# Kernel optimization log

Hardware: AMD Instinct MI355X
Metric: run time of the kernel (lower is better)

Reference implementation:

```python
import jax, jax.numpy as jnp
import numpy as np

B, S, E, H, I = 32, 257, 1024, 16, 4096
D = E // H  # head_dim = 64
EPS = 1e-5


def setup_inputs() -> dict:
    key = jax.random.key(0)
    ks = jax.random.split(key, 12)
    std = 0.02
    inp = {
        'hidden_states': jax.random.normal(ks[0], (B, S, E), jnp.float32),
        'attention_mask': jnp.zeros((B, 1, S, S), jnp.float32),
        'causal_attention_mask': jnp.zeros((B, 1, S, S), jnp.float32),
        'ln1_w': jnp.ones((E,), jnp.float32),
        'ln1_b': jnp.zeros((E,), jnp.float32),
        'q_w': jax.random.normal(ks[1], (E, E), jnp.float32) * std,
        'q_b': jnp.zeros((E,), jnp.float32),
        'k_w': jax.random.normal(ks[2], (E, E), jnp.float32) * std,
        'k_b': jnp.zeros((E,), jnp.float32),
        'v_w': jax.random.normal(ks[3], (E, E), jnp.float32) * std,
        'v_b': jnp.zeros((E,), jnp.float32),
        'o_w': jax.random.normal(ks[4], (E, E), jnp.float32) * std,
        'o_b': jnp.zeros((E,), jnp.float32),
        'ln2_w': jnp.ones((E,), jnp.float32),
        'ln2_b': jnp.zeros((E,), jnp.float32),
        'fc1_w': jax.random.normal(ks[5], (I, E), jnp.float32) * std,
        'fc1_b': jnp.zeros((I,), jnp.float32),
        'fc2_w': jax.random.normal(ks[6], (E, I), jnp.float32) * std,
        'fc2_b': jnp.zeros((E,), jnp.float32),
    }
    return inp


def _layernorm(x, w, b):
    mu = jnp.mean(x, axis=-1, keepdims=True)
    var = jnp.mean(jnp.square(x - mu), axis=-1, keepdims=True)
    return (x - mu) * jax.lax.rsqrt(var + EPS) * w + b


def _gelu_tanh(x):
    # 0.5*x*(1+tanh(sqrt(2/pi)*(x+0.044715*x^3)))
    c = np.sqrt(2.0 / np.pi).astype(np.float32)
    return 0.5 * x * (1.0 + jnp.tanh(c * (x + 0.044715 * x * x * x)))


def reference(hidden_states, attention_mask, causal_attention_mask,
              ln1_w, ln1_b, q_w, q_b, k_w, k_b, v_w, v_b, o_w, o_b,
              ln2_w, ln2_b, fc1_w, fc1_b, fc2_w, fc2_b):
    scale = D ** -0.5
    residual = hidden_states
    x = _layernorm(hidden_states, ln1_w, ln1_b)

    # projections (torch Linear: x @ W.T + b), q pre-scaled as in source
    q = (x @ q_w.T + q_b) * scale
    k = x @ k_w.T + k_b
    v = x @ v_w.T + v_b

    # [B, H, S, D]
    q = q.reshape(B, S, H, D).transpose(0, 2, 1, 3)
    k = k.reshape(B, S, H, D).transpose(0, 2, 1, 3)
    v = v.reshape(B, S, H, D).transpose(0, 2, 1, 3)

    scores = jnp.einsum('bhqd,bhkd->bhqk', q, k)  # [B,H,S,S]
    scores = scores + causal_attention_mask + attention_mask
    probs = jax.nn.softmax(scores, axis=-1)
    ctx = jnp.einsum('bhqk,bhkd->bhqd', probs, v)
    ctx = ctx.transpose(0, 2, 1, 3).reshape(B, S, E)
    attn_out = ctx @ o_w.T + o_b

    h = residual + attn_out
    residual = h
    x = _layernorm(h, ln2_w, ln2_b)
    x = _gelu_tanh(x @ fc1_w.T + fc1_b)
    x = x @ fc2_w.T + fc2_b
    return residual + x
```

## Files before the change

kernel.cpp:

```cpp
#include <hip/hip_runtime.h>

typedef unsigned short u16;
typedef unsigned int   u32;
typedef short s16x8 __attribute__((ext_vector_type(8)));
typedef float f32x4 __attribute__((ext_vector_type(4)));

#define MFMA16(A,B,C) __builtin_amdgcn_mfma_f32_16x16x32_bf16((A),(B),(C),0,0,0)

#define B_   32
#define S_   257
#define E_   1024
#define H_   16
#define D_   64
#define I_   4096
#define M_   (B_*S_)

__device__ __forceinline__ u16 f2bf(float f) {
    u32 u = __float_as_uint(f);
    u32 r = u + 0x7fffu + ((u >> 16) & 1u);
    return (u16)(r >> 16);
}
__device__ __forceinline__ float bf2f(u16 b) {
    return __uint_as_float(((u32)b) << 16);
}

__device__ __forceinline__ void gload16(const void* g, void* l) {
    __builtin_amdgcn_global_load_lds(
        (const __attribute__((address_space(1))) u32*)g,
        (__attribute__((address_space(3))) u32*)l, 16, 0, 0);
}

__global__ __launch_bounds__(256)
void convert_w_kernel(const float* __restrict__ qw, const float* __restrict__ kw,
                      const float* __restrict__ vw, const float* __restrict__ ow,
                      const float* __restrict__ f1, const float* __restrict__ f2,
                      u16* __restrict__ dst)
{
    const int total4 = (12 * 1048576) / 4;
    for (int i = blockIdx.x * 256 + threadIdx.x; i < total4; i += gridDim.x * 256) {
        int e = i * 4;
        int seg = e >> 20;
        const float* srcp; int off;
        if (seg < 4)      { srcp = (seg == 0 ? qw : seg == 1 ? kw : seg == 2 ? vw : ow); off = e & 1048575; }
        else if (seg < 8) { srcp = f1; off = e - 4 * 1048576; }
        else              { srcp = f2; off = e - 8 * 1048576; }
        float4 v = *(const float4*)(srcp + off);
        ushort4 o;
        o.x = f2bf(v.x); o.y = f2bf(v.y); o.z = f2bf(v.z); o.w = f2bf(v.w);
        *(ushort4*)(dst + e) = o;
    }
}

__global__ __launch_bounds__(256)
void mask_combine_kernel(const float* __restrict__ am, const float* __restrict__ cm,
                         u16* __restrict__ msum)
{
    const int total = B_ * S_ * 272;
    for (int i = blockIdx.x * 256 + threadIdx.x; i < total; i += gridDim.x * 256) {
        int skv = i % 272;
        int rem = i / 272;
        int sq  = rem % S_;
        int b   = rem / S_;
        float v;
        if (skv < S_) {
            size_t o = ((size_t)b * S_ + sq) * S_ + skv;
            v = am[o] + cm[o];
        } else v = -1e30f;
        msum[i] = f2bf(v);
    }
}

__global__ __launch_bounds__(256)
void ln_kernel(const float* __restrict__ src, const float* __restrict__ gam,
               const float* __restrict__ bet, u16* __restrict__ dst)
{
    int row = blockIdx.x;
    const float4* p = (const float4*)(src + (size_t)row * E_);
    float4 x = p[threadIdx.x];
    float s  = x.x + x.y + x.z + x.w;
    float s2 = x.x * x.x + x.y * x.y + x.z * x.z + x.w * x.w;
#pragma unroll
    for (int xm = 1; xm < 64; xm <<= 1) {
        s  += __shfl_xor(s,  xm, 64);
        s2 += __shfl_xor(s2, xm, 64);
    }
    __shared__ float red[8];
    int wv = threadIdx.x >> 6;
    if ((threadIdx.x & 63) == 0) { red[wv] = s; red[4 + wv] = s2; }
    __syncthreads();
    s  = red[0] + red[1] + red[2] + red[3];
    s2 = red[4] + red[5] + red[6] + red[7];
    float mu  = s * (1.0f / 1024.0f);
    float var = s2 * (1.0f / 1024.0f) - mu * mu;
    float rs  = rsqrtf(var + 1e-5f);
    float4 g  = ((const float4*)gam)[threadIdx.x];
    float4 be = ((const float4*)bet)[threadIdx.x];
    ushort4 o;
    o.x = f2bf((x.x - mu) * rs * g.x + be.x);
    o.y = f2bf((x.y - mu) * rs * g.y + be.y);
    o.z = f2bf((x.z - mu) * rs * g.z + be.z);
    o.w = f2bf((x.w - mu) * rs * g.w + be.w);
    ((ushort4*)dst)[(size_t)row * 256 + threadIdx.x] = o;
}

template<int MODE>
__global__ __launch_bounds__(256)
void gemm_bt(const u16* __restrict__ A,
             const u16* __restrict__ B0, const u16* __restrict__ B1, const u16* __restrict__ B2,
             const float* __restrict__ bias0, const float* __restrict__ bias1, const float* __restrict__ bias2,
             const float* __restrict__ res, float* __restrict__ outF,
             u16* __restrict__ outB0, u16* __restrict__ outB1, u16* __restrict__ outB2,
             int M, int N, int K)
{
    __shared__ u16 As[128 * 32];
    __shared__ u16 Bs[128 * 32];
    const int tid = threadIdx.x, lane = tid & 63, wv = tid >> 6;
    const int mt = blockIdx.y;
    const u16* Bm = B0; const float* bias = bias0; u16* outB = outB0;
    float scl = 1.0f;
    int nt = blockIdx.x;
    if (MODE == 0) {
        int mat = nt >> 3; nt &= 7;
        if (mat == 1)      { Bm = B1; bias = bias1; outB = outB1; }
        else if (mat == 2) { Bm = B2; bias = bias2; outB = outB2; }
        if (mat == 0) scl = 0.125f;
    }
    const int m0 = mt * 128, n0 = nt * 128;
    const int lr = lane & 15, lg = lane >> 4;
    const int wm = wv >> 1, wn = wv & 1;

    f32x4 acc[4][4];
#pragma unroll
    for (int i = 0; i < 4; ++i)
#pragma unroll
        for (int j = 0; j < 4; ++j) { f32x4 z = {0.f, 0.f, 0.f, 0.f}; acc[i][j] = z; }

    for (int k0 = 0; k0 < K; k0 += 32) {
#pragma unroll
        for (int i = 0; i < 2; ++i) {
            int c  = i * 256 + tid;
            int r  = c >> 2, cc = (c & 3) << 3;
            int ra = m0 + r; if (ra > M - 1) ra = M - 1;
            gload16(A  + (size_t)ra * K + k0 + cc, As + (i * 256 + wv * 64) * 8);
            gload16(Bm + (size_t)(n0 + r) * K + k0 + cc, Bs + (i * 256 + wv * 64) * 8);
        }
        __syncthreads();
        s16x8 af[4], bfr[4];
#pragma unroll
        for (int f = 0; f < 4; ++f) {
            af[f]  = *(const s16x8*)&As[(wm * 64 + f * 16 + lr) * 32 + lg * 8];
            bfr[f] = *(const s16x8*)&Bs[(wn * 64 + f * 16 + lr) * 32 + lg * 8];
        }
#pragma unroll
        for (int fm = 0; fm < 4; ++fm)
#pragma unroll
            for (int fn = 0; fn < 4; ++fn)
                acc[fm][fn] = MFMA16(af[fm], bfr[fn], acc[fm][fn]);
        __syncthreads();
    }

    float biasv[4];
#pragma unroll
    for (int fn = 0; fn < 4; ++fn) biasv[fn] = bias[n0 + wn * 64 + fn * 16 + lr];

#pragma unroll
    for (int fm = 0; fm < 4; ++fm) {
#pragma unroll
        for (int r = 0; r < 4; ++r) {
            int row = m0 + wm * 64 + fm * 16 + lg * 4 + r;
            if (row >= M) continue;
            if (MODE == 0) {
                int bb = row / S_;
                int ss = row - bb * S_;
#pragma unroll
                for (int fn = 0; fn < 4; ++fn) {
                    int col = n0 + wn * 64 + fn * 16 + lr;
                    int hh = col >> 6, dd = col & 63;
                    float v = (acc[fm][fn][r] + biasv[fn]) * scl;
                    outB[(((size_t)bb * H_ + hh) * S_ + ss) * D_ + dd] = f2bf(v);
                }
            } else if (MODE == 1) {
                size_t base = (size_t)row * N;
#pragma unroll
                for (int fn = 0; fn < 4; ++fn) {
                    int col = n0 + wn * 64 + fn * 16 + lr;
                    outF[base + col] = acc[fm][fn][r] + biasv[fn] + res[base + col];
                }
            } else {
                size_t base = (size_t)row * N;
#pragma unroll
                for (int fn = 0; fn < 4; ++fn) {
                    int col = n0 + wn * 64 + fn * 16 + lr;
                    float x = acc[fm][fn][r] + biasv[fn];
                    float u = 0.7978845608028654f * (x + 0.044715f * x * x * x);
                    float t = tanhf(u);
                    outB[base + col] = f2bf(0.5f * x * (1.0f + t));
                }
            }
        }
    }
}

__global__ __launch_bounds__(256)
void attn_kernel(const u16* __restrict__ qg_, const u16* __restrict__ kg_,
                 const u16* __restrict__ vg_, const u16* __restrict__ msum,
                 u16* __restrict__ ctx)
{
    __shared__ u16 Ks[272 * 72];
    __shared__ u16 Vt[64 * 296];
    __shared__ u16 Ps[4][16 * 32];
    const int bh = blockIdx.x;
    const int b = bh >> 4, hh = bh & 15;
    const u16* kg = kg_ + (size_t)bh * (S_ * D_);
    const u16* vg = vg_ + (size_t)bh * (S_ * D_);
    const u16* qg = qg_ + (size_t)bh * (S_ * D_);
    const int tid = threadIdx.x, lane = tid & 63, wv = tid >> 6;

    for (int c = tid; c < (S_ * D_) / 8; c += 256) {
        int s = c >> 3, d8 = (c & 7) << 3;
        s16x8 val = *(const s16x8*)(kg + s * 64 + d8);
        *(s16x8*)&Ks[s * 72 + d8] = val;
    }
    for (int idx = tid; idx < 15 * 64; idx += 256) {
        int rr = 257 + (idx >> 6), cc = idx & 63;
        Ks[rr * 72 + cc] = 0;
    }
    for (int c = tid; c < (S_ * D_) / 8; c += 256) {
        int s = c >> 3, d8 = (c & 7) << 3;
        s16x8 val = *(const s16x8*)(vg + s * 64 + d8);
#pragma unroll
        for (int j = 0; j < 8; ++j) Vt[(d8 + j) * 296 + s] = (u16)val[j];
    }
    for (int idx = tid; idx < 64 * 39; idx += 256) {
        int dd = idx / 39, cc = 257 + idx % 39;
        Vt[dd * 296 + cc] = 0;
    }
    __syncthreads();

    const int lr = lane & 15, lg = lane >> 4;
    for (int qb = wv; qb < 17; qb += 4) {
        const int q0 = qb * 16;
        int qrow = q0 + lr; if (qrow > S_ - 1) qrow = S_ - 1;
        s16x8 aq0 = *(const s16x8*)(qg + qrow * 64 + lg * 8);
        s16x8 aq1 = *(const s16x8*)(qg + qrow * 64 + 32 + lg * 8);

        f32x4 sc[17];
#pragma unroll
        for (int t = 0; t < 17; ++t) { f32x4 z = {0.f, 0.f, 0.f, 0.f}; sc[t] = z; }
#pragma unroll
        for (int t = 0; t < 17; ++t) {
            s16x8 b0 = *(const s16x8*)&Ks[(t * 16 + lr) * 72 + lg * 8];
            s16x8 b1 = *(const s16x8*)&Ks[(t * 16 + lr) * 72 + 32 + lg * 8];
            sc[t] = MFMA16(aq0, b0, sc[t]);
            sc[t] = MFMA16(aq1, b1, sc[t]);
        }
        float mx[4] = {-3e38f, -3e38f, -3e38f, -3e38f};
#pragma unroll
        for (int r = 0; r < 4; ++r) {
            int sq = q0 + lg * 4 + r; if (sq > S_ - 1) sq = S_ - 1;
            const u16* mrow = msum + ((size_t)b * S_ + sq) * 272;
#pragma unroll
            for (int t = 0; t < 17; ++t) {
                sc[t][r] += bf2f(mrow[t * 16 + lr]);
                mx[r] = fmaxf(mx[r], sc[t][r]);
            }
        }
#pragma unroll
        for (int r = 0; r < 4; ++r) {
#pragma unroll
            for (int xm = 1; xm <= 8; xm <<= 1)
                mx[r] = fmaxf(mx[r], __shfl_xor(mx[r], xm, 64));
        }
        float sum[4] = {0.f, 0.f, 0.f, 0.f};
#pragma unroll
        for (int t = 0; t < 17; ++t)
#pragma unroll
            for (int r = 0; r < 4; ++r) {
                float e = __expf(sc[t][r] - mx[r]);
                sc[t][r] = e; sum[r] += e;
            }
#pragma unroll
        for (int r = 0; r < 4; ++r) {
#pragma unroll
            for (int xm = 1; xm <= 8; xm <<= 1)
                sum[r] += __shfl_xor(sum[r], xm, 64);
        }

        f32x4 ac[4];
#pragma unroll
        for (int nt = 0; nt < 4; ++nt) { f32x4 z = {0.f, 0.f, 0.f, 0.f}; ac[nt] = z; }
        u16* myP = &Ps[wv][0];
#pragma unroll
        for (int kc = 0; kc < 9; ++kc) {
#pragma unroll
            for (int tt = 0; tt < 2; ++tt) {
                const int t = kc * 2 + tt;
#pragma unroll
                for (int r = 0; r < 4; ++r) {
                    float pv = (t < 17) ? sc[(t < 17) ? t : 0][r] : 0.f;
                    myP[(lg * 4 + r) * 32 + tt * 16 + lr] = f2bf(pv);
                }
            }
            s16x8 pa = *(const s16x8*)&myP[lr * 32 + lg * 8];
#pragma unroll
            for (int nt = 0; nt < 4; ++nt) {
                s16x8 bv = *(const s16x8*)&Vt[(nt * 16 + lr) * 296 + kc * 32 + lg * 8];
                ac[nt] = MFMA16(pa, bv, ac[nt]);
            }
        }
#pragma unroll
        for (int r = 0; r < 4; ++r) {
            int sq = q0 + lg * 4 + r;
            if (sq < S_) {
                float rd = 1.0f / sum[r];
                size_t base = (((size_t)b * S_ + sq) * H_ + hh) * D_;
#pragma unroll
                for (int nt = 0; nt < 4; ++nt)
                    ctx[base + nt * 16 + lr] = f2bf(ac[nt][r] * rd);
            }
        }
    }
}

extern "C" void kernel_launch(void* const* d_in, const int* in_sizes, int n_in,
                              void* d_out, int out_size, void* d_ws, size_t ws_size,
                              hipStream_t stream)
{
    const float* hid   = (const float*)d_in[0];
    const float* am    = (const float*)d_in[1];
    const float* cm    = (const float*)d_in[2];
    const float* ln1w  = (const float*)d_in[3];
    const float* ln1b  = (const float*)d_in[4];
    const float* qw    = (const float*)d_in[5];
    const float* qbias = (const float*)d_in[6];
    const float* kw    = (const float*)d_in[7];
    const float* kbias = (const float*)d_in[8];
    const float* vw    = (const float*)d_in[9];
    const float* vbias = (const float*)d_in[10];
    const float* ow    = (const float*)d_in[11];
    const float* obias = (const float*)d_in[12];
    const float* ln2w  = (const float*)d_in[13];
    const float* ln2b  = (const float*)d_in[14];
    const float* f1w   = (const float*)d_in[15];
    const float* f1b   = (const float*)d_in[16];
    const float* f2w   = (const float*)d_in[17];
    const float* f2b   = (const float*)d_in[18];
    float* out = (float*)d_out;

    const size_t ME = (size_t)M_ * E_;
    u16* Wq   = (u16*)d_ws;
    u16* Wk   = Wq + 1048576;
    u16* Wv   = Wk + 1048576;
    u16* Wo   = Wv + 1048576;
    u16* Wf1  = Wo + 1048576;
    u16* Wf2  = Wf1 + 4 * 1048576;
    u16* xln  = Wf2 + 4 * 1048576;
    u16* qb_  = xln + ME;
    u16* kb_  = qb_ + ME;
    u16* vb_  = kb_ + ME;
    u16* ctx  = vb_ + ME;
    float* hbuf = (float*)(ctx + ME);
    u16* msum = (u16*)(hbuf + ME);
    u16* act  = qb_;
    u16* x2   = xln;

    convert_w_kernel<<<3072, 256, 0, stream>>>(qw, kw, vw, ow, f1w, f2w, Wq);
    mask_combine_kernel<<<8736, 256, 0, stream>>>(am, cm, msum);
    ln_kernel<<<M_, 256, 0, stream>>>(hid, ln1w, ln1b, xln);
    gemm_bt<0><<<dim3(24, 65), 256, 0, stream>>>(xln, Wq, Wk, Wv, qbias, kbias, vbias,
                                                 nullptr, nullptr, qb_, kb_, vb_,
                                                 M_, E_, E_);
    attn_kernel<<<512, 256, 0, stream>>>(qb_, kb_, vb_, msum, ctx);
    gemm_bt<1><<<dim3(8, 65), 256, 0, stream>>>(ctx, Wo, nullptr, nullptr, obias, nullptr, nullptr,
                                                hid, hbuf, nullptr, nullptr, nullptr,
                                                M_, E_, E_);
    ln_kernel<<<M_, 256, 0, stream>>>(hbuf, ln2w, ln2b, x2);
    gemm_bt<2><<<dim3(32, 65), 256, 0, stream>>>(x2, Wf1, nullptr, nullptr, f1b, nullptr, nullptr,
                                                 nullptr, nullptr, act, nullptr, nullptr,
                                                 M_, I_, E_);
    gemm_bt<1><<<dim3(8, 65), 256, 0, stream>>>(act, Wf2, nullptr, nullptr, f2b, nullptr, nullptr,
                                                hbuf, out, nullptr, nullptr, nullptr,
                                                M_, E_, I_);
}
```

Before: 461.4 us.

## Replace GEMM with 256x256-tile 8-wave kernel using double-buffered swizzled LDS pipeline

Replaces the 128x128 single-buffered GEMM with a 512-thread kernel computing 256x256 tiles. Global-to-LDS loads for the next K step are interleaved with MFMA phases through a double buffer, with explicit waitcnt, barriers and setprio. LDS addresses are XOR-swizzled to cut bank conflicts. The intent is to raise data reuse per load and hide memory latency behind matrix math. In exchange it uses many more registers (32 accumulators per wave) and leaves a coarser grid with more padding waste on the M edge (8224 rows in 33 tiles of 256).

```diff
diff --git a/kernel.cpp b/kernel.cpp
--- a/kernel.cpp
+++ b/kernel.cpp
@@ -6,6 +6,7 @@
 typedef float f32x4 __attribute__((ext_vector_type(4)));
 
 #define MFMA16(A,B,C) __builtin_amdgcn_mfma_f32_16x16x32_bf16((A),(B),(C),0,0,0)
+#define BAR() asm volatile("s_barrier" ::: "memory")
 
 #define B_   32
 #define S_   257
@@ -104,94 +105,159 @@
 }
 
 template<int MODE>
-__global__ __launch_bounds__(256)
-void gemm_bt(const u16* __restrict__ A,
-             const u16* __restrict__ B0, const u16* __restrict__ B1, const u16* __restrict__ B2,
-             const float* __restrict__ bias0, const float* __restrict__ bias1, const float* __restrict__ bias2,
-             const float* __restrict__ res, float* __restrict__ outF,
-             u16* __restrict__ outB0, u16* __restrict__ outB1, u16* __restrict__ outB2,
-             int M, int N, int K)
-{
-    __shared__ u16 As[128 * 32];
-    __shared__ u16 Bs[128 * 32];
-    const int tid = threadIdx.x, lane = tid & 63, wv = tid >> 6;
+__global__ __launch_bounds__(512, 2)
+void gemm8(const u16* __restrict__ A,
+           const u16* __restrict__ Bq, const u16* __restrict__ Bk, const u16* __restrict__ Bv,
+           const float* __restrict__ biasq, const float* __restrict__ biask, const float* __restrict__ biasvv,
+           const float* __restrict__ res, float* __restrict__ outF,
+           u16* __restrict__ outBq, u16* __restrict__ outBk, u16* __restrict__ outBv,
+           int M, int N, int K)
+{
+    __shared__ u16 lds[8][4096];
+    const int tid  = threadIdx.x;
+    const int lane = tid & 63, w = tid >> 6;
+    const int lr = lane & 15, lg = lane >> 4;
+    const int wm = w >> 2, wn = w & 3;
     const int mt = blockIdx.y;
-    const u16* Bm = B0; const float* bias = bias0; u16* outB = outB0;
-    float scl = 1.0f;
-    int nt = blockIdx.x;
+
+    const u16* Bm = Bq; const float* bias = biasq; u16* outB = outBq;
+    float scl = 1.0f; int nt = blockIdx.x;
     if (MODE == 0) {
-        int mat = nt >> 3; nt &= 7;
-        if (mat == 1)      { Bm = B1; bias = bias1; outB = outB1; }
-        else if (mat == 2) { Bm = B2; bias = bias2; outB = outB2; }
+        int mat = nt >> 2; nt &= 3;
+        if (mat == 1)      { Bm = Bk; bias = biask; outB = outBk; }
+        else if (mat == 2) { Bm = Bv; bias = biasvv; outB = outBv; }
         if (mat == 0) scl = 0.125f;
     }
-    const int m0 = mt * 128, n0 = nt * 128;
-    const int lr = lane & 15, lg = lane >> 4;
-    const int wm = wv >> 1, wn = wv & 1;
-
-    f32x4 acc[4][4];
-#pragma unroll
-    for (int i = 0; i < 4; ++i)
+    const int m0 = mt * 256, n0 = nt * 256;
+    const int NT = K >> 5;
+
+    auto STAGE = [&](const u16* g, int grow0, int rowmax, int kt, int mat, int h) {
+        char* dst = (char*)&lds[((kt & 1) << 2) + (mat << 1) + h][0] + w * 1024;
+        int p = (w * 64 + lane) << 4;
+        int l = p ^ (((p >> 7) & 3) << 4);
+        int row = l >> 6, cc = (l >> 4) & 3;
+        int gr = grow0 + row; if (gr > rowmax) gr = rowmax;
+        gload16(g + (size_t)gr * K + (kt << 5) + cc * 8, dst);
+    };
+    const int swv = ((lr >> 1) & 3) << 4;
+    auto LDA = [&](int kt, int mh, int mf) -> s16x8 {
+        const char* base = (const char*)&lds[((kt & 1) << 2) + wm][0];
+        return *(const s16x8*)(base + (mh * 64 + mf * 16 + lr) * 64 + ((lg * 16) ^ swv));
+    };
+    auto LDB = [&](int kt, int nh, int nf) -> s16x8 {
+        const char* base = (const char*)&lds[((kt & 1) << 2) + 2 + (wn >> 1)][0];
+        return *(const s16x8*)(base + ((wn & 1) * 64 + nh * 32 + nf * 16 + lr) * 64 + ((lg * 16) ^ swv));
+    };
+
+    f32x4 acc[8][4];
+#pragma unroll
+    for (int i = 0; i < 8; ++i)
 #pragma unroll
         for (int j = 0; j < 4; ++j) { f32x4 z = {0.f, 0.f, 0.f, 0.f}; acc[i][j] = z; }
 
-    for (int k0 = 0; k0 < K; k0 += 32) {
-#pragma unroll
-        for (int i = 0; i < 2; ++i) {
-            int c  = i * 256 + tid;
-            int r  = c >> 2, cc = (c & 3) << 3;
-            int ra = m0 + r; if (ra > M - 1) ra = M - 1;
-            gload16(A  + (size_t)ra * K + k0 + cc, As + (i * 256 + wv * 64) * 8);
-            gload16(Bm + (size_t)(n0 + r) * K + k0 + cc, Bs + (i * 256 + wv * 64) * 8);
-        }
-        __syncthreads();
-        s16x8 af[4], bfr[4];
-#pragma unroll
-        for (int f = 0; f < 4; ++f) {
-            af[f]  = *(const s16x8*)&As[(wm * 64 + f * 16 + lr) * 32 + lg * 8];
-            bfr[f] = *(const s16x8*)&Bs[(wn * 64 + f * 16 + lr) * 32 + lg * 8];
-        }
-#pragma unroll
-        for (int fm = 0; fm < 4; ++fm)
-#pragma unroll
-            for (int fn = 0; fn < 4; ++fn)
-                acc[fm][fn] = MFMA16(af[fm], bfr[fn], acc[fm][fn]);
-        __syncthreads();
+    STAGE(A,  m0,       M - 1, 0, 0, 0);
+    STAGE(A,  m0 + 128, M - 1, 0, 0, 1);
+    STAGE(Bm, n0,       N - 1, 0, 1, 0);
+    STAGE(Bm, n0 + 128, N - 1, 0, 1, 1);
+    if (NT > 1) {
+        STAGE(A, m0, M - 1, 1, 0, 0);
+        asm volatile("s_waitcnt vmcnt(1)" ::: "memory");
+    } else {
+        asm volatile("s_waitcnt vmcnt(0)" ::: "memory");
+    }
+    BAR();
+
+    s16x8 aq[4], b0q[2], b1q[2];
+    for (int kt = 0; kt < NT; ++kt) {
+#pragma unroll
+        for (int mf = 0; mf < 4; ++mf) aq[mf] = LDA(kt, 0, mf);
+#pragma unroll
+        for (int nf = 0; nf < 2; ++nf) b0q[nf] = LDB(kt, 0, nf);
+        if (kt + 1 < NT) {
+            STAGE(A,  m0 + 128, M - 1, kt + 1, 0, 1);
+            STAGE(Bm, n0,       N - 1, kt + 1, 1, 0);
+        }
+        BAR();
+        __builtin_amdgcn_s_setprio(1);
+#pragma unroll
+        for (int mf = 0; mf < 4; ++mf)
+#pragma unroll
+            for (int nf = 0; nf < 2; ++nf)
+                acc[mf][nf] = MFMA16(aq[mf], b0q[nf], acc[mf][nf]);
+        __builtin_amdgcn_s_setprio(0);
+        BAR();
+#pragma unroll
+        for (int nf = 0; nf < 2; ++nf) b1q[nf] = LDB(kt, 1, nf);
+        if (kt + 1 < NT) STAGE(Bm, n0 + 128, N - 1, kt + 1, 1, 1);
+        BAR();
+        __builtin_amdgcn_s_setprio(1);
+#pragma unroll
+        for (int mf = 0; mf < 4; ++mf)
+#pragma unroll
+            for (int nf = 0; nf < 2; ++nf)
+                acc[mf][2 + nf] = MFMA16(aq[mf], b1q[nf], acc[mf][2 + nf]);
+        __builtin_amdgcn_s_setprio(0);
+        BAR();
+#pragma unroll
+        for (int mf = 0; mf < 4; ++mf) aq[mf] = LDA(kt, 1, mf);
+        BAR();
+        __builtin_amdgcn_s_setprio(1);
+#pragma unroll
+        for (int mf = 0; mf < 4; ++mf)
+#pragma unroll
+            for (int nf = 0; nf < 2; ++nf)
+                acc[4 + mf][2 + nf] = MFMA16(aq[mf], b1q[nf], acc[4 + mf][2 + nf]);
+        __builtin_amdgcn_s_setprio(0);
+        BAR();
+        if (kt + 2 < NT) STAGE(A, m0, M - 1, kt + 2, 0, 0);
+        BAR();
+        __builtin_amdgcn_s_setprio(1);
+#pragma unroll
+        for (int mf = 0; mf < 4; ++mf)
+#pragma unroll
+            for (int nf = 0; nf < 2; ++nf)
+                acc[4 + mf][nf] = MFMA16(aq[mf], b0q[nf], acc[4 + mf][nf]);
+        __builtin_amdgcn_s_setprio(0);
+        if (kt + 1 < NT) {
+            if (kt + 2 < NT) asm volatile("s_waitcnt vmcnt(1)" ::: "memory");
+            else             asm volatile("s_waitcnt vmcnt(0)" ::: "memory");
+        }
+        BAR();
     }
 
     float biasv[4];
 #pragma unroll
-    for (int fn = 0; fn < 4; ++fn) biasv[fn] = bias[n0 + wn * 64 + fn * 16 + lr];
-
-#pragma unroll
-    for (int fm = 0; fm < 4; ++fm) {
+    for (int an = 0; an < 4; ++an) biasv[an] = bias[n0 + wn * 64 + an * 16 + lr];
+
+#pragma unroll
+    for (int am = 0; am < 8; ++am) {
 #pragma unroll
         for (int r = 0; r < 4; ++r) {
-            int row = m0 + wm * 64 + fm * 16 + lg * 4 + r;
+            int row = m0 + wm * 128 + am * 16 + lg * 4 + r;
             if (row >= M) continue;
             if (MODE == 0) {
                 int bb = row / S_;
                 int ss = row - bb * S_;
 #pragma unroll
-                for (int fn = 0; fn < 4; ++fn) {
-                    int col = n0 + wn * 64 + fn * 16 + lr;
+                for (int an = 0; an < 4; ++an) {
+                    int col = n0 + wn * 64 + an * 16 + lr;
                     int hh = col >> 6, dd = col & 63;
-                    float v = (acc[fm][fn][r] + biasv[fn]) * scl;
+                    float v = (acc[am][an][r] + biasv[an]) * scl;
                     outB[(((size_t)bb * H_ + hh) * S_ + ss) * D_ + dd] = f2bf(v);
                 }
             } else if (MODE == 1) {
                 size_t base = (size_t)row * N;
 #pragma unroll
-                for (int fn = 0; fn < 4; ++fn) {
-                    int col = n0 + wn * 64 + fn * 16 + lr;
-                    outF[base + col] = acc[fm][fn][r] + biasv[fn] + res[base + col];
+                for (int an = 0; an < 4; ++an) {
+                    int col = n0 + wn * 64 + an * 16 + lr;
+                    outF[base + col] = acc[am][an][r] + biasv[an] + res[base + col];
                 }
             } else {
                 size_t base = (size_t)row * N;
 #pragma unroll
-                for (int fn = 0; fn < 4; ++fn) {
-                    int col = n0 + wn * 64 + fn * 16 + lr;
-                    float x = acc[fm][fn][r] + biasv[fn];
+                for (int an = 0; an < 4; ++an) {
+                    int col = n0 + wn * 64 + an * 16 + lr;
+                    float x = acc[am][an][r] + biasv[an];
                     float u = 0.7978845608028654f * (x + 0.044715f * x * x * x);
                     float t = tanhf(u);
                     outB[base + col] = f2bf(0.5f * x * (1.0f + t));
@@ -367,18 +433,18 @@
     convert_w_kernel<<<3072, 256, 0, stream>>>(qw, kw, vw, ow, f1w, f2w, Wq);
     mask_combine_kernel<<<8736, 256, 0, stream>>>(am, cm, msum);
     ln_kernel<<<M_, 256, 0, stream>>>(hid, ln1w, ln1b, xln);
-    gemm_bt<0><<<dim3(24, 65), 256, 0, stream>>>(xln, Wq, Wk, Wv, qbias, kbias, vbias,
-                                                 nullptr, nullptr, qb_, kb_, vb_,
-                                                 M_, E_, E_);
+    gemm8<0><<<dim3(12, 33), 512, 0, stream>>>(xln, Wq, Wk, Wv, qbias, kbias, vbias,
+                                               nullptr, nullptr, qb_, kb_, vb_,
+                                               M_, 1024, 1024);
     attn_kernel<<<512, 256, 0, stream>>>(qb_, kb_, vb_, msum, ctx);
-    gemm_bt<1><<<dim3(8, 65), 256, 0, stream>>>(ctx, Wo, nullptr, nullptr, obias, nullptr, nullptr,
-                                                hid, hbuf, nullptr, nullptr, nullptr,
-                                                M_, E_, E_);
+    gemm8<1><<<dim3(4, 33), 512, 0, stream>>>(ctx, Wo, nullptr, nullptr, obias, nullptr, nullptr,
+                                              hid, hbuf, nullptr, nullptr, nullptr,
+                                              M_, 1024, 1024);
     ln_kernel<<<M_, 256, 0, stream>>>(hbuf, ln2w, ln2b, x2);
-    gemm_bt<2><<<dim3(32, 65), 256, 0, stream>>>(x2, Wf1, nullptr, nullptr, f1b, nullptr, nullptr,
-                                                 nullptr, nullptr, act, nullptr, nullptr,
-                                                 M_, I_, E_);
-    gemm_bt<1><<<dim3(8, 65), 256, 0, stream>>>(act, Wf2, nullptr, nullptr, f2b, nullptr, nullptr,
-                                                hbuf, out, nullptr, nullptr, nullptr,
-                                                M_, E_, I_);
-}
+    gemm8<2><<<dim3(16, 33), 512, 0, stream>>>(x2, Wf1, nullptr, nullptr, f1b, nullptr, nullptr,
+                                               nullptr, nullptr, act, nullptr, nullptr,
+                                               M_, 4096, 1024);
+    gemm8<1><<<dim3(4, 33), 512, 0, stream>>>(act, Wf2, nullptr, nullptr, f2b, nullptr, nullptr,
+                                              hbuf, out, nullptr, nullptr, nullptr,
+                                              M_, 1024, 4096);
+}
```

Measured after the change: 464.4 us. Within noise of the previous version (+0.7%).

## Rewrite GEMMs with 256x256 tiles, double-buffered LDS, swizzle and XCD remap

Applied to the files above, without the earlier changes.

Replaces the 128x128 single-buffered GEMM with a 512-thread kernel that uses 256x256 output tiles, prefetches K-tiles two steps ahead into double-buffered LDS with explicit vmcnt waits, and XOR-swizzles LDS addresses to reduce bank conflicts. Workgroup IDs are remapped so that consecutive tiles land on the same XCD, which should improve L2 reuse. The GELU epilogue swaps tanhf for an exp-based sigmoid form. The goal is more data reuse per loaded byte and overlap of global loads with MFMA work, at the cost of higher register pressure and fewer workgroups.

```diff
diff --git a/kernel.cpp b/kernel.cpp
--- a/kernel.cpp
+++ b/kernel.cpp
@@ -6,6 +6,9 @@
 typedef float f32x4 __attribute__((ext_vector_type(4)));
 
 #define MFMA16(A,B,C) __builtin_amdgcn_mfma_f32_16x16x32_bf16((A),(B),(C),0,0,0)
+#define BAR()  asm volatile("s_barrier" ::: "memory")
+#define VMC4   asm volatile("s_waitcnt vmcnt(4)" ::: "memory")
+#define VMC0   asm volatile("s_waitcnt vmcnt(0)" ::: "memory")
 
 #define B_   32
 #define S_   257
@@ -14,6 +17,7 @@
 #define D_   64
 #define I_   4096
 #define M_   (B_*S_)
+#define MT_  33
 
 __device__ __forceinline__ u16 f2bf(float f) {
     u32 u = __float_as_uint(f);
@@ -104,97 +108,137 @@
 }
 
 template<int MODE>
-__global__ __launch_bounds__(256)
-void gemm_bt(const u16* __restrict__ A,
-             const u16* __restrict__ B0, const u16* __restrict__ B1, const u16* __restrict__ B2,
-             const float* __restrict__ bias0, const float* __restrict__ bias1, const float* __restrict__ bias2,
-             const float* __restrict__ res, float* __restrict__ outF,
-             u16* __restrict__ outB0, u16* __restrict__ outB1, u16* __restrict__ outB2,
-             int M, int N, int K)
-{
-    __shared__ u16 As[128 * 32];
-    __shared__ u16 Bs[128 * 32];
-    const int tid = threadIdx.x, lane = tid & 63, wv = tid >> 6;
-    const int mt = blockIdx.y;
-    const u16* Bm = B0; const float* bias = bias0; u16* outB = outB0;
+__global__ __launch_bounds__(512, 4)
+void gemmK(const u16* __restrict__ A,
+           const u16* __restrict__ Bq, const u16* __restrict__ Bk, const u16* __restrict__ Bv,
+           const float* __restrict__ biasq, const float* __restrict__ biask, const float* __restrict__ biasvv,
+           const float* __restrict__ res, float* __restrict__ outF,
+           u16* __restrict__ outBq, u16* __restrict__ outBk, u16* __restrict__ outBv,
+           int M, int N, int K)
+{
+    __shared__ u16 lds[2][4][4096];
+    const int tid = threadIdx.x, lane = tid & 63, w = tid >> 6;
+    const int lr = lane & 15, lg = lane >> 4;
+    const int wm = w >> 2, wn = w & 3;
+
+    const int nwg = gridDim.x;
+    const int q8 = nwg >> 3, r8 = nwg & 7;
+    const int xcd = blockIdx.x & 7, o8 = blockIdx.x >> 3;
+    const int wg = (xcd < r8 ? xcd * (q8 + 1) : r8 * (q8 + 1) + (xcd - r8) * q8) + o8;
+    int nt = wg / MT_;
+    const int mt = wg - nt * MT_;
+
+    const u16* Bm = Bq; const float* bias = biasq; u16* outB = outBq;
     float scl = 1.0f;
-    int nt = blockIdx.x;
     if (MODE == 0) {
-        int mat = nt >> 3; nt &= 7;
-        if (mat == 1)      { Bm = B1; bias = bias1; outB = outB1; }
-        else if (mat == 2) { Bm = B2; bias = bias2; outB = outB2; }
+        int mat = nt >> 2; nt &= 3;
+        if (mat == 1)      { Bm = Bk; bias = biask; outB = outBk; }
+        else if (mat == 2) { Bm = Bv; bias = biasvv; outB = outBv; }
         if (mat == 0) scl = 0.125f;
     }
-    const int m0 = mt * 128, n0 = nt * 128;
-    const int lr = lane & 15, lg = lane >> 4;
-    const int wm = wv >> 1, wn = wv & 1;
-
-    f32x4 acc[4][4];
-#pragma unroll
-    for (int i = 0; i < 4; ++i)
+    const int m0 = mt * 256, n0 = nt * 256;
+    const int NTt = K >> 5;
+
+    const int p    = tid * 16;
+    const int l_   = p ^ (((p >> 7) & 3) << 4);
+    const int srow = l_ >> 6;
+    const int scol = (l_ & 63) >> 1;
+
+    auto STAGE4 = [&](int buf, int t) {
+        const int kc = t << 5;
+        {   int gr = m0 + srow;       if (gr > M - 1) gr = M - 1;
+            gload16(A  + (size_t)gr * K + kc + scol, (char*)&lds[buf][0][0] + p); }
+        {   int gr = m0 + 128 + srow; if (gr > M - 1) gr = M - 1;
+            gload16(A  + (size_t)gr * K + kc + scol, (char*)&lds[buf][1][0] + p); }
+        {   int gr = n0 + srow;       if (gr > N - 1) gr = N - 1;
+            gload16(Bm + (size_t)gr * K + kc + scol, (char*)&lds[buf][2][0] + p); }
+        {   int gr = n0 + 128 + srow; if (gr > N - 1) gr = N - 1;
+            gload16(Bm + (size_t)gr * K + kc + scol, (char*)&lds[buf][3][0] + p); }
+    };
+    auto LDA = [&](int buf, int mh, int mf) -> s16x8 {
+        const char* b = (const char*)&lds[buf][wm][0];
+        int inrow = mh * 64 + mf * 16 + lr;
+        return *(const s16x8*)(b + inrow * 64 + ((lg * 16) ^ (((inrow >> 1) & 3) << 4)));
+    };
+    auto LDB = [&](int buf, int nf) -> s16x8 {
+        const char* b = (const char*)&lds[buf][2 + (wn >> 1)][0];
+        int inrow = (wn & 1) * 64 + nf * 16 + lr;
+        return *(const s16x8*)(b + inrow * 64 + ((lg * 16) ^ (((inrow >> 1) & 3) << 4)));
+    };
+
+    f32x4 acc[8][4];
+#pragma unroll
+    for (int i = 0; i < 8; ++i)
 #pragma unroll
         for (int j = 0; j < 4; ++j) { f32x4 z = {0.f, 0.f, 0.f, 0.f}; acc[i][j] = z; }
 
-    for (int k0 = 0; k0 < K; k0 += 32) {
-#pragma unroll
-        for (int i = 0; i < 2; ++i) {
-            int c  = i * 256 + tid;
-            int r  = c >> 2, cc = (c & 3) << 3;
-            int ra = m0 + r; if (ra > M - 1) ra = M - 1;
-            gload16(A  + (size_t)ra * K + k0 + cc, As + (i * 256 + wv * 64) * 8);
-            gload16(Bm + (size_t)(n0 + r) * K + k0 + cc, Bs + (i * 256 + wv * 64) * 8);
-        }
-        __syncthreads();
-        s16x8 af[4], bfr[4];
-#pragma unroll
-        for (int f = 0; f < 4; ++f) {
-            af[f]  = *(const s16x8*)&As[(wm * 64 + f * 16 + lr) * 32 + lg * 8];
-            bfr[f] = *(const s16x8*)&Bs[(wn * 64 + f * 16 + lr) * 32 + lg * 8];
-        }
-#pragma unroll
-        for (int fm = 0; fm < 4; ++fm)
-#pragma unroll
-            for (int fn = 0; fn < 4; ++fn)
-                acc[fm][fn] = MFMA16(af[fm], bfr[fn], acc[fm][fn]);
-        __syncthreads();
+    STAGE4(0, 0);
+    STAGE4(1, 1);
+    VMC4;
+    BAR();
+
+    for (int t = 0; t < NTt; ++t) {
+        const int cur = t & 1;
+        s16x8 bf[4];
+#pragma unroll
+        for (int nf = 0; nf < 4; ++nf) bf[nf] = LDB(cur, nf);
+#pragma unroll
+        for (int mh = 0; mh < 2; ++mh) {
+            s16x8 af[4];
+#pragma unroll
+            for (int mf = 0; mf < 4; ++mf) af[mf] = LDA(cur, mh, mf);
+#pragma unroll
+            for (int mf = 0; mf < 4; ++mf)
+#pragma unroll
+                for (int nf = 0; nf < 4; ++nf)
+                    acc[mh * 4 + mf][nf] = MFMA16(af[mf], bf[nf], acc[mh * 4 + mf][nf]);
+        }
+        BAR();
+        if (t + 2 < NTt) STAGE4(cur, t + 2);
+        if (t + 1 < NTt) {
+            if (t + 2 < NTt) { VMC4; } else { VMC0; }
+        }
+        BAR();
     }
 
     float biasv[4];
 #pragma unroll
-    for (int fn = 0; fn < 4; ++fn) biasv[fn] = bias[n0 + wn * 64 + fn * 16 + lr];
-
-#pragma unroll
-    for (int fm = 0; fm < 4; ++fm) {
+    for (int nf = 0; nf < 4; ++nf)
+        biasv[nf] = bias[n0 + wn * 64 + nf * 16 + lr];
+
+#pragma unroll
+    for (int am = 0; am < 8; ++am) {
 #pragma unroll
         for (int r = 0; r < 4; ++r) {
-            int row = m0 + wm * 64 + fm * 16 + lg * 4 + r;
+            int row = m0 + wm * 128 + (am >> 2) * 64 + (am & 3) * 16 + lg * 4 + r;
             if (row >= M) continue;
             if (MODE == 0) {
                 int bb = row / S_;
                 int ss = row - bb * S_;
 #pragma unroll
-                for (int fn = 0; fn < 4; ++fn) {
-                    int col = n0 + wn * 64 + fn * 16 + lr;
+                for (int nf = 0; nf < 4; ++nf) {
+                    int col = n0 + wn * 64 + nf * 16 + lr;
                     int hh = col >> 6, dd = col & 63;
-                    float v = (acc[fm][fn][r] + biasv[fn]) * scl;
+                    float v = (acc[am][nf][r] + biasv[nf]) * scl;
                     outB[(((size_t)bb * H_ + hh) * S_ + ss) * D_ + dd] = f2bf(v);
                 }
             } else if (MODE == 1) {
                 size_t base = (size_t)row * N;
 #pragma unroll
-                for (int fn = 0; fn < 4; ++fn) {
-                    int col = n0 + wn * 64 + fn * 16 + lr;
-                    outF[base + col] = acc[fm][fn][r] + biasv[fn] + res[base + col];
+                for (int nf = 0; nf < 4; ++nf) {
+                    int col = n0 + wn * 64 + nf * 16 + lr;
+                    outF[base + col] = acc[am][nf][r] + biasv[nf] + res[base + col];
                 }
             } else {
                 size_t base = (size_t)row * N;
 #pragma unroll
-                for (int fn = 0; fn < 4; ++fn) {
-                    int col = n0 + wn * 64 + fn * 16 + lr;
-                    float x = acc[fm][fn][r] + biasv[fn];
-                    float u = 0.7978845608028654f * (x + 0.044715f * x * x * x);
-                    float t = tanhf(u);
-                    outB[base + col] = f2bf(0.5f * x * (1.0f + t));
+                for (int nf = 0; nf < 4; ++nf) {
+                    int col = n0 + wn * 64 + nf * 16 + lr;
+                    float x = acc[am][nf][r] + biasv[nf];
+                    float u2 = 1.5957691216057308f * (x + 0.044715f * x * x * x);
+                    u2 = fminf(u2, 80.0f);
+                    float tt = __expf(u2);
+                    outB[base + col] = f2bf(x * tt / (1.0f + tt));
                 }
             }
         }
@@ -367,18 +411,18 @@
     convert_w_kernel<<<3072, 256, 0, stream>>>(qw, kw, vw, ow, f1w, f2w, Wq);
     mask_combine_kernel<<<8736, 256, 0, stream>>>(am, cm, msum);
     ln_kernel<<<M_, 256, 0, stream>>>(hid, ln1w, ln1b, xln);
-    gemm_bt<0><<<dim3(24, 65), 256, 0, stream>>>(xln, Wq, Wk, Wv, qbias, kbias, vbias,
-                                                 nullptr, nullptr, qb_, kb_, vb_,
-                                                 M_, E_, E_);
+    gemmK<0><<<12 * MT_, 512, 0, stream>>>(xln, Wq, Wk, Wv, qbias, kbias, vbias,
+                                           nullptr, nullptr, qb_, kb_, vb_,
+                                           M_, 1024, 1024);
     attn_kernel<<<512, 256, 0, stream>>>(qb_, kb_, vb_, msum, ctx);
-    gemm_bt<1><<<dim3(8, 65), 256, 0, stream>>>(ctx, Wo, nullptr, nullptr, obias, nullptr, nullptr,
-                                                hid, hbuf, nullptr, nullptr, nullptr,
-                                                M_, E_, E_);
+    gemmK<1><<<4 * MT_, 512, 0, stream>>>(ctx, Wo, nullptr, nullptr, obias, nullptr, nullptr,
+                                          hid, hbuf, nullptr, nullptr, nullptr,
+                                          M_, 1024, 1024);
     ln_kernel<<<M_, 256, 0, stream>>>(hbuf, ln2w, ln2b, x2);
-    gemm_bt<2><<<dim3(32, 65), 256, 0, stream>>>(x2, Wf1, nullptr, nullptr, f1b, nullptr, nullptr,
-                                                 nullptr, nullptr, act, nullptr, nullptr,
-                                                 M_, I_, E_);
-    gemm_bt<1><<<dim3(8, 65), 256, 0, stream>>>(act, Wf2, nullptr, nullptr, f2b, nullptr, nullptr,
-                                                hbuf, out, nullptr, nullptr, nullptr,
-                                                M_, E_, I_);
-}
+    gemmK<2><<<16 * MT_, 512, 0, stream>>>(x2, Wf1, nullptr, nullptr, f1b, nullptr, nullptr,
+                                           nullptr, nullptr, act, nullptr, nullptr,
+                                           M_, 4096, 1024);
+    gemmK<1><<<4 * MT_, 512, 0, stream>>>(act, Wf2, nullptr, nullptr, f2b, nullptr, nullptr,
+                                          hbuf, out, nullptr, nullptr, nullptr,
+                                          M_, 1024, 4096);
+}
```

Result: slower. 1.649 ms (+257.4%).
